# Kernel tuning notes

Hardware: AMD Instinct MI355X
Metric: run time of the kernel (lower is better)

## Reference

```python
import jax, jax.numpy as jnp
import numpy as np

TEMPERATURE = 0.1  # InfoNCE default
K_POS, K_NEG = 5, 10


def _l2norm(x, eps):
    return x / jnp.maximum(jnp.linalg.norm(x, axis=-1, keepdims=True), eps)


def setup_inputs() -> dict:
    key = jax.random.key(0)
    k1, k2 = jax.random.split(key)
    anchor = jax.random.normal(k1, (4096, 512), dtype=jnp.float32)
    sample = jax.random.normal(k2, (4096, 512), dtype=jnp.float32)
    return {"anchor": anchor, "sample": sample}


def reference(anchor, sample):
    N = anchor.shape[0]
    # Pairwise cosine similarity (torch.cosine_similarity eps=1e-8), computed
    a = _l2norm(anchor, 1e-8)
    sim = a @ a.T  # (N, N)

    # topk largest=True (5 nearest) and largest=False (10 farthest)
    _, pos_idx = jax.lax.top_k(sim, K_POS)    # (N, 5)
    _, neg_idx = jax.lax.top_k(-sim, K_NEG)   # (N, 10), ascending sim

    # Faithful replication of the original gather/repeat pattern:
    # query = sample.repeat(5, 1) -> tiling (index i maps to sample[i % N])
    query = jnp.tile(sample, (K_POS, 1))                          # (5N, d)
    pos = sample[pos_idx.reshape(-1)]                             # (5N, d) anchor-major
    neg = sample[neg_idx.reshape(-1)].reshape(N, K_NEG, -1)       # (N, 10, d)
    neg = jnp.repeat(neg, K_POS, axis=0)                          # (5N, 10, d)

    # InfoNCE (negative_mode='paired'): F.normalize (eps=1e-12) then logits.
    q = _l2norm(query, 1e-12)
    p = _l2norm(pos, 1e-12)
    n = _l2norm(neg, 1e-12)
    pos_logit = jnp.sum(q * p, axis=1, keepdims=True)             # (5N, 1)
    neg_logits = jnp.einsum('bd,bkd->bk', q, n)                   # (5N, 10)
    logits = jnp.concatenate([pos_logit, neg_logits], axis=1) / TEMPERATURE
    # cross_entropy with labels == 0, mean reduction
    loss = -jnp.mean(jax.nn.log_softmax(logits, axis=1)[:, 0])
    return loss
```

## Files before the change

### kernel.cpp

```cpp
#include <hip/hip_runtime.h>
#include <math.h>

#define N 4096
#define D 512
#define KPOS 5
#define KNEG 10
#define NB 32
#define NPAIR (NB * (NB - 1) / 2)
#define NJOB 1024

typedef short s16x8 __attribute__((ext_vector_type(8)));
typedef unsigned short u16x8 __attribute__((ext_vector_type(8)));
typedef float f32x4 __attribute__((ext_vector_type(4)));

__device__ __forceinline__ unsigned short f2bf(float x) {
    unsigned u = __float_as_uint(x);
    unsigned r = (u + 0x7FFFu + ((u >> 16) & 1u)) >> 16;
    return (unsigned short)r;
}
__device__ __forceinline__ float bf2f(unsigned short b) {
    return __uint_as_float(((unsigned)b) << 16);
}
__device__ __forceinline__ unsigned umax_(unsigned a, unsigned b) { return a > b ? a : b; }
__device__ __forceinline__ unsigned umin_(unsigned a, unsigned b) { return a < b ? a : b; }

__global__ __launch_bounds__(256) void norm_kernel(const float* __restrict__ anchor,
                                                   const float* __restrict__ sample,
                                                   unsigned short* __restrict__ Abf,
                                                   unsigned short* __restrict__ s_norm) {
    const int wave = threadIdx.x >> 6, lane = threadIdx.x & 63;
    const int row = blockIdx.x * 4 + wave;
    const bool is_anchor = row < N;
    const float* in = is_anchor ? anchor + (size_t)row * D
                                : sample + (size_t)(row - N) * D;
    const float eps = is_anchor ? 1e-8f : 1e-12f;

    float v[8];
    float ss = 0.f;
#pragma unroll
    for (int e = 0; e < 8; ++e) {
        v[e] = in[lane + 64 * e];
        ss = fmaf(v[e], v[e], ss);
    }
#pragma unroll
    for (int off = 32; off > 0; off >>= 1) ss += __shfl_xor(ss, off);
    const float denom = fmaxf(sqrtf(ss), eps);

    unsigned short* out = is_anchor ? Abf + (size_t)row * D
                                    : s_norm + (size_t)(row - N) * D;
#pragma unroll
    for (int e = 0; e < 8; ++e) out[lane + 64 * e] = f2bf(v[e] / denom);
}

#define ATILE (128 * 64)
#define BTILE (64 * 64)

__device__ __forceinline__ void stage_ab(const unsigned short* __restrict__ A,
                                         unsigned short* As, unsigned short* Bs,
                                         int rowA, int colB, int kl, int t) {
#pragma unroll
    for (int i = 0; i < 4; ++i) {
        const int c = i * 256 + t;
        const int r = c >> 3;
        const int ke = ((c & 7) ^ (r & 7)) * 8;
        __builtin_amdgcn_global_load_lds(
            (const __attribute__((address_space(1))) void*)(A + (size_t)(rowA + r) * D + kl + ke),
            (__attribute__((address_space(3))) void*)(As + c * 8), 16, 0, 0);
    }
#pragma unroll
    for (int i = 0; i < 2; ++i) {
        const int c = i * 256 + t;
        const int r = c >> 3;
        const int ke = ((c & 7) ^ (r & 7)) * 8;
        __builtin_amdgcn_global_load_lds(
            (const __attribute__((address_space(1))) void*)(A + (size_t)(colB + r) * D + kl + ke),
            (__attribute__((address_space(3))) void*)(Bs + c * 8), 16, 0, 0);
    }
}

__global__ __launch_bounds__(256) void gemm_bf16(const unsigned short* __restrict__ Abf,
                                                 unsigned short* __restrict__ C) {
    const int q = (blockIdx.x % 8) * (NJOB / 8) + blockIdx.x / 8;

    int bi, bj, h;
    if (q < 2 * NPAIR) {
        const int op = q >> 1;
        h = q & 1;
        bi = (int)(31.5f - sqrtf(31.5f * 31.5f - 2.f * (float)op));
        while (31 * bi - bi * (bi - 1) / 2 > op) --bi;
        while (31 * (bi + 1) - (bi + 1) * bi / 2 <= op) ++bi;
        bj = bi + 1 + (op - (31 * bi - bi * (bi - 1) / 2));
    } else {
        const int d = q - 2 * NPAIR;
        bi = bj = d >> 1;
        h = d & 1;
    }

    __shared__ __align__(16) unsigned short As[2 * ATILE];
    __shared__ __align__(16) unsigned short Bs[2 * BTILE];

    const int t = threadIdx.x;
    const int l = t & 63;
    const int w = t >> 6;
    const int wr = w >> 1, wc = w & 1;
    const int rowA = bi * 128;
    const int colB = bj * 128 + h * 64;
    const int lrow = l & 15, lgrp = l >> 4;

    f32x4 acc[4][2];
#pragma unroll
    for (int m = 0; m < 4; ++m)
#pragma unroll
        for (int n = 0; n < 2; ++n) acc[m][n] = (f32x4){0.f, 0.f, 0.f, 0.f};

    stage_ab(Abf, As, Bs, rowA, colB, 0, t);
    __syncthreads();

    for (int kc = 0; kc < 8; ++kc) {
        const int cur = kc & 1;
        if (kc < 7)
            stage_ab(Abf, As + (cur ^ 1) * ATILE, Bs + (cur ^ 1) * BTILE,
                     rowA, colB, (kc + 1) * 64, t);

        const char* AsB = (const char*)(As + cur * ATILE);
        const char* BsB = (const char*)(Bs + cur * BTILE);
#pragma unroll
        for (int kk = 0; kk < 2; ++kk) {
            s16x8 af[4], bfr[2];
#pragma unroll
            for (int m = 0; m < 4; ++m) {
                const int row = wr * 64 + m * 16 + lrow;
                af[m] = *(const s16x8*)(AsB + row * 128 + (((kk * 4 + lgrp) ^ (row & 7)) * 16));
            }
#pragma unroll
            for (int n = 0; n < 2; ++n) {
                const int row = wc * 32 + n * 16 + lrow;
                bfr[n] = *(const s16x8*)(BsB + row * 128 + (((kk * 4 + lgrp) ^ (row & 7)) * 16));
            }
#pragma unroll
            for (int m = 0; m < 4; ++m)
#pragma unroll
                for (int n = 0; n < 2; ++n)
                    acc[m][n] = __builtin_amdgcn_mfma_f32_16x16x32_bf16(af[m], bfr[n], acc[m][n], 0, 0, 0);
        }
        __syncthreads();
    }

#pragma unroll
    for (int m = 0; m < 4; ++m) {
#pragma unroll
        for (int n = 0; n < 2; ++n) {
            const int col = colB + wc * 32 + n * 16 + lrow;
            const int row0 = rowA + wr * 64 + m * 16 + lgrp * 4;
#pragma unroll
            for (int j = 0; j < 4; ++j)
                C[(size_t)(row0 + j) * N + col] = f2bf(acc[m][n][j]);
        }
    }
    if (bi != bj) {
#pragma unroll
        for (int m = 0; m < 4; ++m) {
#pragma unroll
            for (int n = 0; n < 2; ++n) {
                const int col = colB + wc * 32 + n * 16 + lrow;
                const int row0 = rowA + wr * 64 + m * 16 + lgrp * 4;
                ushort4 pk;
                pk.x = f2bf(acc[m][n][0]);
                pk.y = f2bf(acc[m][n][1]);
                pk.z = f2bf(acc[m][n][2]);
                pk.w = f2bf(acc[m][n][3]);
                *(ushort4*)&C[(size_t)col * N + row0] = pk;
            }
        }
    }
}

__global__ __launch_bounds__(256) void fused_topk_loss(const unsigned short* __restrict__ sim,
                                                       const unsigned short* __restrict__ s_norm,
                                                       float* __restrict__ partials) {
    __shared__ float wsum[4];
    const int wave = threadIdx.x >> 6, lane = threadIdx.x & 63;
    const int ia = blockIdx.x * 4 + wave;
    const unsigned short* s = sim + (size_t)ia * N;
    const int cc = lane & 15;
    const int g = lane >> 4;

    unsigned tk[KPOS], bk[KNEG];
#pragma unroll
    for (int qq = 0; qq < KPOS; ++qq) tk[qq] = 0u;
#pragma unroll
    for (int qq = 0; qq < KNEG; ++qq) bk[qq] = 0xFFFFFFFFu;

    for (int e = 0; e < 8; ++e) {
        const int base = 8 * (lane + 64 * e);
        const u16x8 v8 = *(const u16x8*)&s[base];
#pragma unroll
        for (int j = 0; j < 8; ++j) {
            unsigned u = ((unsigned)v8[j]) << 16;
            u ^= ((unsigned)((int)u >> 31)) | 0x80000000u;
            const unsigned kv = u & 0xFFFF0000u;
            const int idx = base + j;

            unsigned c = kv | (unsigned)(4095 - idx);
#pragma unroll
            for (int qq = 0; qq < KPOS - 1; ++qq) {
                const unsigned x = umax_(tk[qq], c);
                c = umin_(tk[qq], c);
                tk[qq] = x;
            }
            tk[KPOS - 1] = umax_(tk[KPOS - 1], c);

            c = kv | (unsigned)idx;
#pragma unroll
            for (int qq = 0; qq < KNEG - 1; ++qq) {
                const unsigned x = umin_(bk[qq], c);
                c = umax_(bk[qq], c);
                bk[qq] = x;
            }
            bk[KNEG - 1] = umax_(bk[KNEG - 1], c);
        }
    }

    int rowB = 0;
#pragma unroll
    for (int it = 0; it < KPOS; ++it) {
        unsigned m = tk[0];
#pragma unroll
        for (int off = 32; off > 0; off >>= 1) m = umax_(m, (unsigned)__shfl_xor((int)m, off));
        const int widx = 4095 - (int)(m & 0xFFFu);
        if (cc == it) rowB = widx;
        if (tk[0] == m) {
#pragma unroll
            for (int qq = 0; qq < KPOS - 1; ++qq) tk[qq] = tk[qq + 1];
            tk[KPOS - 1] = 0u;
        }
    }
#pragma unroll
    for (int it = 0; it < KNEG; ++it) {
        unsigned m = bk[0];
#pragma unroll
        for (int off = 32; off > 0; off >>= 1) m = umin_(m, (unsigned)__shfl_xor((int)m, off));
        const int widx = (int)(m & 0xFFFu);
        if (cc == KPOS + it) rowB = widx;
        if (bk[0] == m) {
#pragma unroll
            for (int qq = 0; qq < KNEG - 1; ++qq) bk[qq] = bk[qq + 1];
            bk[KNEG - 1] = 0xFFFFFFFFu;
        }
    }

    const int rowA = (ia * KPOS + ((cc < KPOS) ? cc : 0)) & (N - 1);
    const unsigned short* pA = s_norm + (size_t)rowA * D + g * 8;
    const unsigned short* pB = s_norm + (size_t)rowB * D + g * 8;

    s16x8 a[16], b[16];
#pragma unroll
    for (int kk = 0; kk < 16; ++kk) {
        a[kk] = *(const s16x8*)(pA + kk * 32);
        b[kk] = *(const s16x8*)(pB + kk * 32);
    }
    f32x4 acc = (f32x4){0.f, 0.f, 0.f, 0.f};
#pragma unroll
    for (int kk = 0; kk < 16; ++kk)
        acc = __builtin_amdgcn_mfma_f32_16x16x32_bf16(a[kk], b[kk], acc, 0, 0, 0);

    float lsum = 0.f;
#pragma unroll
    for (int j = 0; j < 4; ++j) {
        const int p = g * 4 + j;
        const float logit = acc[j] * 10.f;
        const bool isneg = (cc >= KPOS) && (cc < 15);
        const bool ispos = (cc == p);
        float x = (ispos || isneg) ? logit : -__builtin_inff();
        float m = x;
#pragma unroll
        for (int off = 1; off < 16; off <<= 1) m = fmaxf(m, __shfl_xor(m, off));
        float e = (ispos || isneg) ? expf(logit - m) : 0.f;
        float sx = e;
#pragma unroll
        for (int off = 1; off < 16; off <<= 1) sx += __shfl_xor(sx, off);
        float l0 = ispos ? logit : 0.f;
#pragma unroll
        for (int off = 1; off < 16; off <<= 1) l0 += __shfl_xor(l0, off);
        if (p < KPOS && ispos) lsum += logf(sx) + m - l0;
    }

#pragma unroll
    for (int off = 32; off > 0; off >>= 1) lsum += __shfl_xor(lsum, off);
    if (lane == 0) wsum[wave] = lsum;
    __syncthreads();
    if (threadIdx.x == 0)
        partials[blockIdx.x] = wsum[0] + wsum[1] + wsum[2] + wsum[3];
}

__global__ __launch_bounds__(256) void reduce_kernel(const float* __restrict__ partials,
                                                     float* __restrict__ out) {
    __shared__ float wsum[4];
    const int wave = threadIdx.x >> 6, lane = threadIdx.x & 63;
    float s = partials[threadIdx.x] + partials[threadIdx.x + 256] +
              partials[threadIdx.x + 512] + partials[threadIdx.x + 768];
#pragma unroll
    for (int off = 32; off > 0; off >>= 1) s += __shfl_xor(s, off);
    if (lane == 0) wsum[wave] = s;
    __syncthreads();
    if (threadIdx.x == 0)
        *out = (wsum[0] + wsum[1] + wsum[2] + wsum[3]) * (1.0f / (float)(N * KPOS));
}

extern "C" void kernel_launch(void* const* d_in, const int* in_sizes, int n_in,
                              void* d_out, int out_size, void* d_ws, size_t ws_size,
                              hipStream_t stream) {
    const float* anchor = (const float*)d_in[0];
    const float* sample = (const float*)d_in[1];
    float* out = (float*)d_out;

    char* ws = (char*)d_ws;
    unsigned short* Abf    = (unsigned short*)ws;
    unsigned short* s_norm = (unsigned short*)(ws + (size_t)4 * 1024 * 1024);
    unsigned short* sim    = (unsigned short*)(ws + (size_t)8 * 1024 * 1024);
    float* partials = (float*)(ws + (size_t)40 * 1024 * 1024);

    norm_kernel<<<2048, 256, 0, stream>>>(anchor, sample, Abf, s_norm);

    gemm_bf16<<<NJOB, 256, 0, stream>>>(Abf, sim);

    fused_topk_loss<<<N / 4, 256, 0, stream>>>(sim, s_norm, partials);

    reduce_kernel<<<1, 256, 0, stream>>>(partials, out);
}
```

Before: 62.51 us.

## Pre-map sim to sortable keys in GEMM and fuse final reduction via atomic ticket

The GEMM epilogue now stores each bf16 similarity already converted to a monotone unsigned sort key. The top-k loop therefore skips the per-element sign-flip transform and only shifts the value into place. The separate single-block reduce kernel is removed: the last block of the top-k/loss kernel, chosen with an atomic ticket counter that norm_kernel resets, sums the partials and writes the loss. This saves one kernel launch and some ALU work per element, at the cost of an atomic and a fence in every block.

```diff
diff --git a/kernel.cpp b/kernel.cpp
--- a/kernel.cpp
+++ b/kernel.cpp
@@ -21,13 +21,19 @@
 __device__ __forceinline__ float bf2f(unsigned short b) {
     return __uint_as_float(((unsigned)b) << 16);
 }
+__device__ __forceinline__ unsigned short mapbf(float x) {
+    const unsigned short h = f2bf(x);
+    return h ^ ((h & 0x8000u) ? 0xFFFFu : 0x8000u);
+}
 __device__ __forceinline__ unsigned umax_(unsigned a, unsigned b) { return a > b ? a : b; }
 __device__ __forceinline__ unsigned umin_(unsigned a, unsigned b) { return a < b ? a : b; }
 
 __global__ __launch_bounds__(256) void norm_kernel(const float* __restrict__ anchor,
                                                    const float* __restrict__ sample,
                                                    unsigned short* __restrict__ Abf,
-                                                   unsigned short* __restrict__ s_norm) {
+                                                   unsigned short* __restrict__ s_norm,
+                                                   unsigned* __restrict__ counter) {
+    if (blockIdx.x == 0 && threadIdx.x == 0) *counter = 0u;
     const int wave = threadIdx.x >> 6, lane = threadIdx.x & 63;
     const int row = blockIdx.x * 4 + wave;
     const bool is_anchor = row < N;
@@ -154,7 +160,7 @@
             const int row0 = rowA + wr * 64 + m * 16 + lgrp * 4;
 #pragma unroll
             for (int j = 0; j < 4; ++j)
-                C[(size_t)(row0 + j) * N + col] = f2bf(acc[m][n][j]);
+                C[(size_t)(row0 + j) * N + col] = mapbf(acc[m][n][j]);
         }
     }
     if (bi != bj) {
@@ -165,10 +171,10 @@
                 const int col = colB + wc * 32 + n * 16 + lrow;
                 const int row0 = rowA + wr * 64 + m * 16 + lgrp * 4;
                 ushort4 pk;
-                pk.x = f2bf(acc[m][n][0]);
-                pk.y = f2bf(acc[m][n][1]);
-                pk.z = f2bf(acc[m][n][2]);
-                pk.w = f2bf(acc[m][n][3]);
+                pk.x = mapbf(acc[m][n][0]);
+                pk.y = mapbf(acc[m][n][1]);
+                pk.z = mapbf(acc[m][n][2]);
+                pk.w = mapbf(acc[m][n][3]);
                 *(ushort4*)&C[(size_t)col * N + row0] = pk;
             }
         }
@@ -177,8 +183,11 @@
 
 __global__ __launch_bounds__(256) void fused_topk_loss(const unsigned short* __restrict__ sim,
                                                        const unsigned short* __restrict__ s_norm,
-                                                       float* __restrict__ partials) {
+                                                       float* __restrict__ partials,
+                                                       unsigned* __restrict__ counter,
+                                                       float* __restrict__ out) {
     __shared__ float wsum[4];
+    __shared__ int lastflag;
     const int wave = threadIdx.x >> 6, lane = threadIdx.x & 63;
     const int ia = blockIdx.x * 4 + wave;
     const unsigned short* s = sim + (size_t)ia * N;
@@ -196,9 +205,7 @@
         const u16x8 v8 = *(const u16x8*)&s[base];
 #pragma unroll
         for (int j = 0; j < 8; ++j) {
-            unsigned u = ((unsigned)v8[j]) << 16;
-            u ^= ((unsigned)((int)u >> 31)) | 0x80000000u;
-            const unsigned kv = u & 0xFFFF0000u;
+            const unsigned kv = ((unsigned)v8[j]) << 16;
             const int idx = base + j;
 
             unsigned c = kv | (unsigned)(4095 - idx);
@@ -289,22 +296,26 @@
     for (int off = 32; off > 0; off >>= 1) lsum += __shfl_xor(lsum, off);
     if (lane == 0) wsum[wave] = lsum;
     __syncthreads();
-    if (threadIdx.x == 0)
+    if (threadIdx.x == 0) {
         partials[blockIdx.x] = wsum[0] + wsum[1] + wsum[2] + wsum[3];
-}
-
-__global__ __launch_bounds__(256) void reduce_kernel(const float* __restrict__ partials,
-                                                     float* __restrict__ out) {
-    __shared__ float wsum[4];
-    const int wave = threadIdx.x >> 6, lane = threadIdx.x & 63;
-    float s = partials[threadIdx.x] + partials[threadIdx.x + 256] +
-              partials[threadIdx.x + 512] + partials[threadIdx.x + 768];
-#pragma unroll
-    for (int off = 32; off > 0; off >>= 1) s += __shfl_xor(s, off);
-    if (lane == 0) wsum[wave] = s;
+        __threadfence();
+        const unsigned tkt = atomicAdd(counter, 1u);
+        lastflag = (tkt == (unsigned)(gridDim.x - 1));
+    }
     __syncthreads();
-    if (threadIdx.x == 0)
-        *out = (wsum[0] + wsum[1] + wsum[2] + wsum[3]) * (1.0f / (float)(N * KPOS));
+
+    if (lastflag) {
+        float sacc = 0.f;
+#pragma unroll
+        for (int i = 0; i < 4; ++i)
+            sacc += atomicAdd(&partials[threadIdx.x + 256 * i], 0.f);
+#pragma unroll
+        for (int off = 32; off > 0; off >>= 1) sacc += __shfl_xor(sacc, off);
+        if (lane == 0) wsum[wave] = sacc;
+        __syncthreads();
+        if (threadIdx.x == 0)
+            *out = (wsum[0] + wsum[1] + wsum[2] + wsum[3]) * (1.0f / (float)(N * KPOS));
+    }
 }
 
 extern "C" void kernel_launch(void* const* d_in, const int* in_sizes, int n_in,
@@ -319,12 +330,11 @@
     unsigned short* s_norm = (unsigned short*)(ws + (size_t)4 * 1024 * 1024);
     unsigned short* sim    = (unsigned short*)(ws + (size_t)8 * 1024 * 1024);
     float* partials = (float*)(ws + (size_t)40 * 1024 * 1024);
-
-    norm_kernel<<<2048, 256, 0, stream>>>(anchor, sample, Abf, s_norm);
+    unsigned* counter = (unsigned*)(ws + (size_t)40 * 1024 * 1024 + 4096);
+
+    norm_kernel<<<2048, 256, 0, stream>>>(anchor, sample, Abf, s_norm, counter);
 
     gemm_bf16<<<NJOB, 256, 0, stream>>>(Abf, sim);
 
-    fused_topk_loss<<<N / 4, 256, 0, stream>>>(sim, s_norm, partials);
-
-    reduce_kernel<<<1, 256, 0, stream>>>(partials, out);
-}
+    fused_topk_loss<<<N / 4, 256, 0, stream>>>(sim, s_norm, partials, counter, out);
+}
```

New measurement: 85.31 us. 36.5% more time.

## Split top-k from loss kernel, pre-map sim keys in GEMM, dual top-k chains

Applied to the files above, without the earlier changes.

The GEMM epilogue now stores similarities as order-preserving unsigned keys, so the top-k scan drops its per-element sign flip. The fused top-k/loss kernel is split into a top-k kernel, which keeps two independent insertion chains per lane to expose ILP and then merges them, and a loss kernel that reads the indices from global memory. A sched_barrier is added after the operand loads in the loss kernel. The split adds one kernel launch and a small index round-trip through memory in exchange for shorter dependency chains and lower register pressure per kernel.

```diff
diff --git a/kernel.cpp b/kernel.cpp
--- a/kernel.cpp
+++ b/kernel.cpp
@@ -20,6 +20,10 @@
 }
 __device__ __forceinline__ float bf2f(unsigned short b) {
     return __uint_as_float(((unsigned)b) << 16);
+}
+__device__ __forceinline__ unsigned short mapbf(float x) {
+    const unsigned short h = f2bf(x);
+    return h ^ ((h & 0x8000u) ? 0xFFFFu : 0x8000u);
 }
 __device__ __forceinline__ unsigned umax_(unsigned a, unsigned b) { return a > b ? a : b; }
 __device__ __forceinline__ unsigned umin_(unsigned a, unsigned b) { return a < b ? a : b; }
@@ -154,7 +158,7 @@
             const int row0 = rowA + wr * 64 + m * 16 + lgrp * 4;
 #pragma unroll
             for (int j = 0; j < 4; ++j)
-                C[(size_t)(row0 + j) * N + col] = f2bf(acc[m][n][j]);
+                C[(size_t)(row0 + j) * N + col] = mapbf(acc[m][n][j]);
         }
     }
     if (bi != bj) {
@@ -165,91 +169,113 @@
                 const int col = colB + wc * 32 + n * 16 + lrow;
                 const int row0 = rowA + wr * 64 + m * 16 + lgrp * 4;
                 ushort4 pk;
-                pk.x = f2bf(acc[m][n][0]);
-                pk.y = f2bf(acc[m][n][1]);
-                pk.z = f2bf(acc[m][n][2]);
-                pk.w = f2bf(acc[m][n][3]);
+                pk.x = mapbf(acc[m][n][0]);
+                pk.y = mapbf(acc[m][n][1]);
+                pk.z = mapbf(acc[m][n][2]);
+                pk.w = mapbf(acc[m][n][3]);
                 *(ushort4*)&C[(size_t)col * N + row0] = pk;
             }
         }
     }
 }
 
-__global__ __launch_bounds__(256) void fused_topk_loss(const unsigned short* __restrict__ sim,
-                                                       const unsigned short* __restrict__ s_norm,
-                                                       float* __restrict__ partials) {
+__device__ __forceinline__ void ins_top(unsigned* tk, unsigned c) {
+#pragma unroll
+    for (int q = 0; q < KPOS - 1; ++q) {
+        const unsigned x = umax_(tk[q], c);
+        c = umin_(tk[q], c);
+        tk[q] = x;
+    }
+    tk[KPOS - 1] = umax_(tk[KPOS - 1], c);
+}
+__device__ __forceinline__ void ins_bot(unsigned* bk, unsigned c) {
+#pragma unroll
+    for (int q = 0; q < KNEG - 1; ++q) {
+        const unsigned x = umin_(bk[q], c);
+        c = umax_(bk[q], c);
+        bk[q] = x;
+    }
+    bk[KNEG - 1] = umin_(bk[KNEG - 1], c);
+}
+__device__ __forceinline__ void scan8(const unsigned short* __restrict__ s,
+                                      int lane, int e, unsigned* tk, unsigned* bk) {
+    const int base = 8 * (lane + 64 * e);
+    const u16x8 v8 = *(const u16x8*)&s[base];
+#pragma unroll
+    for (int j = 0; j < 8; ++j) {
+        const unsigned kv = ((unsigned)v8[j]) << 16;
+        const int idx = base + j;
+        ins_top(tk, kv | (unsigned)(idx ^ 0xFFF));
+        ins_bot(bk, kv | (unsigned)idx);
+    }
+}
+
+__global__ __launch_bounds__(256) void topk_kernel(const unsigned short* __restrict__ sim,
+                                                   int* __restrict__ pos_idx,
+                                                   int* __restrict__ neg_idx) {
+    const int w = threadIdx.x >> 6, l = threadIdx.x & 63;
+    const int row = blockIdx.x * 4 + w;
+    const unsigned short* s = sim + (size_t)row * N;
+
+    unsigned tkA[KPOS], bkA[KNEG], tkB[KPOS], bkB[KNEG];
+#pragma unroll
+    for (int q = 0; q < KPOS; ++q) { tkA[q] = 0u; tkB[q] = 0u; }
+#pragma unroll
+    for (int q = 0; q < KNEG; ++q) { bkA[q] = 0xFFFFFFFFu; bkB[q] = 0xFFFFFFFFu; }
+
+#pragma unroll
+    for (int ee = 0; ee < 4; ++ee) {
+        scan8(s, l, 2 * ee, tkA, bkA);
+        scan8(s, l, 2 * ee + 1, tkB, bkB);
+    }
+#pragma unroll
+    for (int q = 0; q < KPOS; ++q) ins_top(tkA, tkB[q]);
+#pragma unroll
+    for (int q = 0; q < KNEG; ++q) ins_bot(bkA, bkB[q]);
+
+#pragma unroll
+    for (int it = 0; it < KPOS; ++it) {
+        unsigned m = tkA[0];
+#pragma unroll
+        for (int off = 32; off > 0; off >>= 1) m = umax_(m, (unsigned)__shfl_xor((int)m, off));
+        if (l == 0) pos_idx[row * KPOS + it] = (int)((m & 0xFFFu) ^ 0xFFFu);
+        if (tkA[0] == m) {
+#pragma unroll
+            for (int q = 0; q < KPOS - 1; ++q) tkA[q] = tkA[q + 1];
+            tkA[KPOS - 1] = 0u;
+        }
+    }
+#pragma unroll
+    for (int it = 0; it < KNEG; ++it) {
+        unsigned m = bkA[0];
+#pragma unroll
+        for (int off = 32; off > 0; off >>= 1) m = umin_(m, (unsigned)__shfl_xor((int)m, off));
+        if (l == 0) neg_idx[row * KNEG + it] = (int)(m & 0xFFFu);
+        if (bkA[0] == m) {
+#pragma unroll
+            for (int q = 0; q < KNEG - 1; ++q) bkA[q] = bkA[q + 1];
+            bkA[KNEG - 1] = 0xFFFFFFFFu;
+        }
+    }
+}
+
+__global__ __launch_bounds__(256) void loss_kernel(const unsigned short* __restrict__ s_norm,
+                                                   const int* __restrict__ pos_idx,
+                                                   const int* __restrict__ neg_idx,
+                                                   float* __restrict__ partials) {
     __shared__ float wsum[4];
     const int wave = threadIdx.x >> 6, lane = threadIdx.x & 63;
     const int ia = blockIdx.x * 4 + wave;
-    const unsigned short* s = sim + (size_t)ia * N;
     const int cc = lane & 15;
     const int g = lane >> 4;
 
-    unsigned tk[KPOS], bk[KNEG];
-#pragma unroll
-    for (int qq = 0; qq < KPOS; ++qq) tk[qq] = 0u;
-#pragma unroll
-    for (int qq = 0; qq < KNEG; ++qq) bk[qq] = 0xFFFFFFFFu;
-
-    for (int e = 0; e < 8; ++e) {
-        const int base = 8 * (lane + 64 * e);
-        const u16x8 v8 = *(const u16x8*)&s[base];
-#pragma unroll
-        for (int j = 0; j < 8; ++j) {
-            unsigned u = ((unsigned)v8[j]) << 16;
-            u ^= ((unsigned)((int)u >> 31)) | 0x80000000u;
-            const unsigned kv = u & 0xFFFF0000u;
-            const int idx = base + j;
-
-            unsigned c = kv | (unsigned)(4095 - idx);
-#pragma unroll
-            for (int qq = 0; qq < KPOS - 1; ++qq) {
-                const unsigned x = umax_(tk[qq], c);
-                c = umin_(tk[qq], c);
-                tk[qq] = x;
-            }
-            tk[KPOS - 1] = umax_(tk[KPOS - 1], c);
-
-            c = kv | (unsigned)idx;
-#pragma unroll
-            for (int qq = 0; qq < KNEG - 1; ++qq) {
-                const unsigned x = umin_(bk[qq], c);
-                c = umax_(bk[qq], c);
-                bk[qq] = x;
-            }
-            bk[KNEG - 1] = umax_(bk[KNEG - 1], c);
-        }
-    }
-
-    int rowB = 0;
-#pragma unroll
-    for (int it = 0; it < KPOS; ++it) {
-        unsigned m = tk[0];
-#pragma unroll
-        for (int off = 32; off > 0; off >>= 1) m = umax_(m, (unsigned)__shfl_xor((int)m, off));
-        const int widx = 4095 - (int)(m & 0xFFFu);
-        if (cc == it) rowB = widx;
-        if (tk[0] == m) {
-#pragma unroll
-            for (int qq = 0; qq < KPOS - 1; ++qq) tk[qq] = tk[qq + 1];
-            tk[KPOS - 1] = 0u;
-        }
-    }
-#pragma unroll
-    for (int it = 0; it < KNEG; ++it) {
-        unsigned m = bk[0];
-#pragma unroll
-        for (int off = 32; off > 0; off >>= 1) m = umin_(m, (unsigned)__shfl_xor((int)m, off));
-        const int widx = (int)(m & 0xFFFu);
-        if (cc == KPOS + it) rowB = widx;
-        if (bk[0] == m) {
-#pragma unroll
-            for (int qq = 0; qq < KNEG - 1; ++qq) bk[qq] = bk[qq + 1];
-            bk[KNEG - 1] = 0xFFFFFFFFu;
-        }
-    }
-
-    const int rowA = (ia * KPOS + ((cc < KPOS) ? cc : 0)) & (N - 1);
+    const int qbase = ia * KPOS;
+    const int rowA = (qbase + ((cc < KPOS) ? cc : 0)) & (N - 1);
+    int rowB;
+    if (cc < KPOS)      rowB = pos_idx[qbase + cc];
+    else if (cc < 15)   rowB = neg_idx[ia * KNEG + (cc - KPOS)];
+    else                rowB = pos_idx[qbase];
+
     const unsigned short* pA = s_norm + (size_t)rowA * D + g * 8;
     const unsigned short* pB = s_norm + (size_t)rowB * D + g * 8;
 
@@ -259,6 +285,9 @@
         a[kk] = *(const s16x8*)(pA + kk * 32);
         b[kk] = *(const s16x8*)(pB + kk * 32);
     }
+    __builtin_amdgcn_sched_barrier(0);
+    asm volatile("" ::: "memory");
+
     f32x4 acc = (f32x4){0.f, 0.f, 0.f, 0.f};
 #pragma unroll
     for (int kk = 0; kk < 16; ++kk)
@@ -318,13 +347,17 @@
     unsigned short* Abf    = (unsigned short*)ws;
     unsigned short* s_norm = (unsigned short*)(ws + (size_t)4 * 1024 * 1024);
     unsigned short* sim    = (unsigned short*)(ws + (size_t)8 * 1024 * 1024);
-    float* partials = (float*)(ws + (size_t)40 * 1024 * 1024);
+    int* pos_idx  = (int*)(ws + (size_t)40 * 1024 * 1024);
+    int* neg_idx  = (int*)(ws + (size_t)40 * 1024 * 1024 + 128 * 1024);
+    float* partials = (float*)(ws + (size_t)41 * 1024 * 1024);
 
     norm_kernel<<<2048, 256, 0, stream>>>(anchor, sample, Abf, s_norm);
 
     gemm_bf16<<<NJOB, 256, 0, stream>>>(Abf, sim);
 
-    fused_topk_loss<<<N / 4, 256, 0, stream>>>(sim, s_norm, partials);
+    topk_kernel<<<N / 4, 256, 0, stream>>>(sim, pos_idx, neg_idx);
+
+    loss_kernel<<<N / 4, 256, 0, stream>>>(s_norm, pos_idx, neg_idx, partials);
 
     reduce_kernel<<<1, 256, 0, stream>>>(partials, out);
 }
```

After: 71.01 us. 1.14x slower.
